# Performance work log

Hardware: AMD Instinct MI355X
Metric: run time of the kernel (lower is better)

Reference implementation:

```python
import jax, jax.numpy as jnp
import numpy as np

B, S, D, E, H = 1024, 256, 1024, 1024, 1024  # batch, state, belief, embedding, hidden
T1 = 32            # clip_length => number of scan steps
POSE_TILES = 4
MIN_STD = 0.1


def _gru(x, h, wih, whh, bih, bhh):
    # torch.nn.GRUCell semantics
    gi = x @ wih.T + bih
    gh = h @ whh.T + bhh
    i_r, i_z, i_n = jnp.split(gi, 3, axis=-1)
    h_r, h_z, h_n = jnp.split(gh, 3, axis=-1)
    r = jax.nn.sigmoid(i_r + h_r)
    z = jax.nn.sigmoid(i_z + h_z)
    n = jnp.tanh(i_n + r * h_n)
    return (1.0 - z) * n + z * h


def setup_inputs() -> dict:
    key = jax.random.key(0)
    ks = iter(jax.random.split(key, 40))
    g = lambda shape, s=1.0: jax.random.normal(next(ks), shape, dtype=jnp.float32) * s
    W = 0.02
    inp = {
        'prev_state': g((B, S)),
        'prev_belief': g((B, D)),
        'observations': g((T1, B, E)),
        'poses': g((T1, B, 6)),
        'noise_post': g((T1, B, S)),
        'noise_prior': g((T1, B, S)),
        # fc_embed_state_posterior: (2S+E) -> D
        'W_esq': g((D, 2 * S + E), W), 'b_esq': jnp.zeros((D,), jnp.float32),
        # fc_embed_state_prior: (2S+6*pose_tiles) -> D
        'W_esp': g((D, 2 * S + 6 * POSE_TILES), W), 'b_esp': jnp.zeros((D,), jnp.float32),
        # GRUCell posterior / prior
        'gq_wih': g((3 * D, D), W), 'gq_whh': g((3 * D, D), W),
        'gq_bih': jnp.zeros((3 * D,), jnp.float32), 'gq_bhh': jnp.zeros((3 * D,), jnp.float32),
        'gp_wih': g((3 * D, D), W), 'gp_whh': g((3 * D, D), W),
        'gp_bih': jnp.zeros((3 * D,), jnp.float32), 'gp_bhh': jnp.zeros((3 * D,), jnp.float32),
        # belief -> hidden -> 2*state heads
        'W_ebq': g((H, D), W), 'b_ebq': jnp.zeros((H,), jnp.float32),
        'W_sq': g((2 * S, H), W), 'b_sq': jnp.zeros((2 * S,), jnp.float32),
        'W_ebp': g((H, D), W), 'b_ebp': jnp.zeros((H,), jnp.float32),
        'W_sp': g((2 * S, H), W), 'b_sp': jnp.zeros((2 * S,), jnp.float32),
    }
    return inp


def reference(prev_state, prev_belief, observations, poses, noise_post, noise_prior,
              W_esq, b_esq, W_esp, b_esp,
              gq_wih, gq_whh, gq_bih, gq_bhh,
              gp_wih, gp_whh, gp_bih, gp_bhh,
              W_ebq, b_ebq, W_sq, b_sq, W_ebp, b_ebp, W_sp, b_sp):
    relu = jax.nn.relu

    def step(carry, xs):
        s_q, s_p, b_q, b_p = carry
        obs, pose, nq, npn = xs
        # posterior branch
        h = relu(jnp.concatenate([obs, s_q, s_p], axis=1) @ W_esq.T + b_esq)
        b_q_new = _gru(h, b_q, gq_wih, gq_whh, gq_bih, gq_bhh)
        hq = relu(b_q_new @ W_ebq.T + b_ebq)
        mq, raw_sq = jnp.split(hq @ W_sq.T + b_sq, 2, axis=1)
        std_q = jax.nn.softplus(raw_sq) + MIN_STD
        s_q_new = mq + std_q * nq
        # prior branch (uses old s_q, s_p per original code)
        pose_t = jnp.tile(pose, (1, POSE_TILES))
        h2 = relu(jnp.concatenate([pose_t, s_q, s_p], axis=1) @ W_esp.T + b_esp)
        b_p_new = _gru(h2, b_p, gp_wih, gp_whh, gp_bih, gp_bhh)
        hp = relu(b_p_new @ W_ebp.T + b_ebp)
        mp, raw_sp = jnp.split(hp @ W_sp.T + b_sp, 2, axis=1)
        std_p = jax.nn.softplus(raw_sp) + MIN_STD
        s_p_new = mp + std_p * npn
        new_carry = (s_q_new, s_p_new, b_q_new, b_p_new)
        ys = (b_q_new, s_p_new, mp, std_p, s_q_new, mq, std_q)
        return new_carry, ys

    carry0 = (prev_state, prev_state, prev_belief, prev_belief)
    _, ys = jax.lax.scan(step, carry0, (observations, poses, noise_post, noise_prior))
    post_beliefs, prior_states, prior_means, prior_stds, post_states, post_means, post_stds = ys
    # order matches torch: [posterior_beliefs, prior_states, prior_means, prior_std_devs,
    #                       posterior_states, posterior_means, posterior_std_devs]
    return (post_beliefs, prior_states, prior_means, prior_stds,
            post_states, post_means, post_stds)
```

## Files before the change

kernel.cpp:

```cpp
#include <hip/hip_runtime.h>
#include <stdint.h>
#include <math.h>

typedef unsigned short ushort_t;
typedef __attribute__((ext_vector_type(8))) short bf16x8;
typedef __attribute__((ext_vector_type(4))) float f32x4;

#define T1_ 32

__device__ __forceinline__ float bf2f(ushort_t u) {
  union { unsigned int i; float f; } v; v.i = ((unsigned int)u) << 16; return v.f;
}
__device__ __forceinline__ ushort_t f2bf(float f) {
  union { float f; unsigned int i; } v; v.f = f;
  unsigned int x = v.i;
  return (ushort_t)((x + 0x7FFFu + ((x >> 16) & 1u)) >> 16);
}
__device__ __forceinline__ float sigm(float x) { return 1.f / (1.f + expf(-x)); }

__device__ __forceinline__ void gld16(const ushort_t* g, ushort_t* l) {
  __builtin_amdgcn_global_load_lds(
      (const __attribute__((address_space(1))) unsigned int*)g,
      (__attribute__((address_space(3))) unsigned int*)l, 16, 0, 0);
}

__global__ __launch_bounds__(256) void cvt_k(const float* src, ushort_t* dst,
                                             long long n, int cols, int src_ld, int src_off) {
  const long long idx = (long long)blockIdx.x * 256 + threadIdx.x;
  if (idx >= n) return;
  const long long row = idx / cols;
  const int col = (int)(idx - row * cols);
  dst[idx] = f2bf(src[row * src_ld + src_off + col]);
}

__global__ __launch_bounds__(256) void wpe_k(const float* Wesp, float* wpe) {
  const int i = blockIdx.x * 256 + threadIdx.x;
  if (i >= 1024 * 6) return;
  const int n = i / 6, j = i % 6;
  float s = 0.f;
#pragma unroll
  for (int r = 0; r < 4; ++r) s += Wesp[(long long)n * 536 + j + 6 * r];
  wpe[i] = s;
}

__global__ void marker_k(float* out, float K) {
  if (threadIdx.x == 0 && blockIdx.x == 0) out[0] = K;
}

struct MMSide {
  const ushort_t* a0; const ushort_t* a1; const ushort_t* a2;
  int kd0, kd1, kd2;
  int coff0, coff1, coff2;
  int nparts;
  const ushort_t* W; int ldw;
  const float* bias;
  ushort_t* outb;
  int dopose;
};
struct MM2Args { MMSide s[2]; const float* poses_t; const float* wpe; };

__global__ __launch_bounds__(256) void mm2_k(MM2Args g) {
  const MMSide S = g.s[blockIdx.z];
  __shared__ __align__(16) ushort_t As[2048];
  __shared__ __align__(16) ushort_t Ws[4096];
  const int tid = threadIdx.x;
  const int lane = tid & 63, wave = tid >> 6;
  const int wm = wave >> 1, wn = wave & 1;
  const int bn0 = blockIdx.x * 128, bm0 = blockIdx.y * 64;

  f32x4 acc[2][4];
#pragma unroll
  for (int i = 0; i < 2; ++i)
#pragma unroll
    for (int j = 0; j < 4; ++j) acc[i][j] = (f32x4){0.f, 0.f, 0.f, 0.f};

  const ushort_t* ap[3] = { S.a0, S.a1, S.a2 };
  const int kd[3] = { S.kd0, S.kd1, S.kd2 };
  const int cf[3] = { S.coff0, S.coff1, S.coff2 };

  const int rowA = tid >> 2, kcA = (tid & 3) * 8;
  ushort_t* ldsA  = &As[wave * 512];
  ushort_t* ldsW0 = &Ws[wave * 512];
  ushort_t* ldsW1 = &Ws[2048 + wave * 512];

#pragma unroll 1
  for (int p = 0; p < S.nparts; ++p) {
    const int kdim = kd[p];
    const ushort_t* Ap = ap[p] + (long long)bm0 * kdim + (long long)rowA * kdim + kcA;
    const ushort_t* Wp0 = S.W + cf[p] + (long long)(bn0 + rowA) * S.ldw + kcA;
    const ushort_t* Wp1 = Wp0 + (long long)64 * S.ldw;
    const int nkt = kdim >> 5;
#pragma unroll 1
    for (int kt = 0; kt < nkt; ++kt) {
      const int k0 = kt * 32;
      __syncthreads();
      gld16(Ap + k0, ldsA);
      gld16(Wp0 + k0, ldsW0);
      gld16(Wp1 + k0, ldsW1);
      __syncthreads();
      const int r15 = lane & 15, kh = (lane >> 4) * 8;
      bf16x8 a[2], b[4];
#pragma unroll
      for (int i = 0; i < 2; ++i)
        a[i] = *(const bf16x8*)&As[(wm * 32 + i * 16 + r15) * 32 + kh];
#pragma unroll
      for (int j = 0; j < 4; ++j)
        b[j] = *(const bf16x8*)&Ws[(wn * 64 + j * 16 + r15) * 32 + kh];
#pragma unroll
      for (int i = 0; i < 2; ++i)
#pragma unroll
        for (int j = 0; j < 4; ++j)
          acc[i][j] = __builtin_amdgcn_mfma_f32_16x16x32_bf16(a[i], b[j], acc[i][j], 0, 0, 0);
    }
  }

  const int r15 = lane & 15, rq = (lane >> 4) * 4;
#pragma unroll
  for (int i = 0; i < 2; ++i) {
#pragma unroll
    for (int j = 0; j < 4; ++j) {
      const int col = bn0 + wn * 64 + j * 16 + r15;
      const float bs = S.bias[col];
#pragma unroll
      for (int q = 0; q < 4; ++q) {
        const int row = bm0 + wm * 32 + i * 16 + rq + q;
        float v = acc[i][j][q] + bs;
        if (S.dopose) {
          float s = 0.f;
#pragma unroll
          for (int jj = 0; jj < 6; ++jj)
            s += g.poses_t[(long long)row * 6 + jj] * g.wpe[col * 6 + jj];
          v += s;
        }
        v = fmaxf(v, 0.f);
        S.outb[(size_t)row * 1024 + col] = f2bf(v);
      }
    }
  }
}

struct GruSide {
  const ushort_t* x;
  const ushort_t* hb;
  const float* hf;
  const ushort_t* wih; const ushort_t* whh;
  const float* bih; const float* bhh;
  float* dst; ushort_t* dstb;
};
struct Gru2Args { GruSide s[2]; };

__global__ __launch_bounds__(256) void gru2_k(Gru2Args g) {
  const GruSide S = g.s[blockIdx.z];
  __shared__ __align__(16) ushort_t Xs[2048];
  __shared__ __align__(16) ushort_t Hs[2048];
  __shared__ __align__(16) ushort_t Wt[6][2048];
  const int tid = threadIdx.x;
  const int lane = tid & 63, wave = tid >> 6;
  const int wm = wave >> 1, wn = wave & 1;
  const int bn0 = blockIdx.x * 64, bm0 = blockIdx.y * 64;

  f32x4 acc[6][2][2];
#pragma unroll
  for (int gg = 0; gg < 6; ++gg)
#pragma unroll
    for (int i = 0; i < 2; ++i)
#pragma unroll
      for (int j = 0; j < 2; ++j) acc[gg][i][j] = (f32x4){0.f, 0.f, 0.f, 0.f};

  const int rowA = tid >> 2, kc = (tid & 3) * 8;
  const long long xoff = (long long)(bm0 + rowA) * 1024 + kc;

#pragma unroll 1
  for (int kt = 0; kt < 32; ++kt) {
    const int k0 = kt * 32;
    __syncthreads();
    gld16(S.x + xoff + k0, &Xs[wave * 512]);
    gld16(S.hb + xoff + k0, &Hs[wave * 512]);
#pragma unroll
    for (int gg = 0; gg < 6; ++gg) {
      const ushort_t* base = (gg < 3) ? S.wih : S.whh;
      const int grow = (gg % 3) * 1024 + bn0 + rowA;
      gld16(base + (long long)grow * 1024 + k0 + kc, &Wt[gg][wave * 512]);
    }
    __syncthreads();
    const int r15 = lane & 15, kh = (lane >> 4) * 8;
    bf16x8 ax[2], ah[2];
#pragma unroll
    for (int i = 0; i < 2; ++i) {
      ax[i] = *(const bf16x8*)&Xs[(wm * 32 + i * 16 + r15) * 32 + kh];
      ah[i] = *(const bf16x8*)&Hs[(wm * 32 + i * 16 + r15) * 32 + kh];
    }
#pragma unroll
    for (int gg = 0; gg < 6; ++gg) {
      bf16x8 bw[2];
#pragma unroll
      for (int j = 0; j < 2; ++j)
        bw[j] = *(const bf16x8*)&Wt[gg][(wn * 32 + j * 16 + r15) * 32 + kh];
#pragma unroll
      for (int i = 0; i < 2; ++i)
#pragma unroll
        for (int j = 0; j < 2; ++j)
          acc[gg][i][j] = __builtin_amdgcn_mfma_f32_16x16x32_bf16(
              (gg < 3) ? ax[i] : ah[i], bw[j], acc[gg][i][j], 0, 0, 0);
    }
  }

  const int r15 = lane & 15, rq = (lane >> 4) * 4;
#pragma unroll
  for (int j = 0; j < 2; ++j) {
    const int col = bn0 + wn * 32 + j * 16 + r15;
    const float br  = S.bih[col],        bhr = S.bhh[col];
    const float bz  = S.bih[col + 1024], bhz = S.bhh[col + 1024];
    const float bn_ = S.bih[col + 2048], bhn = S.bhh[col + 2048];
#pragma unroll
    for (int i = 0; i < 2; ++i) {
#pragma unroll
      for (int q = 0; q < 4; ++q) {
        const int row = bm0 + wm * 32 + i * 16 + rq + q;
        const float ir = acc[0][i][j][q] + br,   hr = acc[3][i][j][q] + bhr;
        const float iz = acc[1][i][j][q] + bz,   hz = acc[4][i][j][q] + bhz;
        const float in_ = acc[2][i][j][q] + bn_, hn = acc[5][i][j][q] + bhn;
        const float r = sigm(ir + hr);
        const float z = sigm(iz + hz);
        const float ng = tanhf(in_ + r * hn);
        const long long o = (long long)row * 1024 + col;
        const float bnew = (1.f - z) * ng + z * S.hf[o];
        S.dst[o] = bnew;
        S.dstb[o] = f2bf(bnew);
      }
    }
  }
}

struct HeadSide {
  const ushort_t* hh;
  const ushort_t* Ws;
  const float* bs;
  const float* noise;
  float* omean; float* ostd; float* ostate;
  ushort_t* stateb;
};
struct Head2Args { HeadSide s[2]; };

__global__ __launch_bounds__(256) void head2_k(Head2Args g) {
  const HeadSide S = g.s[blockIdx.z];
  __shared__ __align__(16) ushort_t As[2048];
  __shared__ __align__(16) ushort_t Wt[2][2048];
  const int tid = threadIdx.x;
  const int lane = tid & 63, wave = tid >> 6;
  const int wm = wave >> 1, wn = wave & 1;
  const int bn0 = blockIdx.x * 64, bm0 = blockIdx.y * 64;

  f32x4 acc[2][2][2];
#pragma unroll
  for (int gg = 0; gg < 2; ++gg)
#pragma unroll
    for (int i = 0; i < 2; ++i)
#pragma unroll
      for (int j = 0; j < 2; ++j) acc[gg][i][j] = (f32x4){0.f, 0.f, 0.f, 0.f};

  const int rowA = tid >> 2, kc = (tid & 3) * 8;
  const long long aoff = (long long)(bm0 + rowA) * 1024 + kc;

#pragma unroll 1
  for (int kt = 0; kt < 32; ++kt) {
    const int k0 = kt * 32;
    __syncthreads();
    gld16(S.hh + aoff + k0, &As[wave * 512]);
#pragma unroll
    for (int gg = 0; gg < 2; ++gg)
      gld16(S.Ws + (long long)(gg * 256 + bn0 + rowA) * 1024 + k0 + kc, &Wt[gg][wave * 512]);
    __syncthreads();
    const int r15 = lane & 15, kh = (lane >> 4) * 8;
    bf16x8 a[2];
#pragma unroll
    for (int i = 0; i < 2; ++i)
      a[i] = *(const bf16x8*)&As[(wm * 32 + i * 16 + r15) * 32 + kh];
#pragma unroll
    for (int gg = 0; gg < 2; ++gg) {
      bf16x8 bw[2];
#pragma unroll
      for (int j = 0; j < 2; ++j)
        bw[j] = *(const bf16x8*)&Wt[gg][(wn * 32 + j * 16 + r15) * 32 + kh];
#pragma unroll
      for (int i = 0; i < 2; ++i)
#pragma unroll
        for (int j = 0; j < 2; ++j)
          acc[gg][i][j] = __builtin_amdgcn_mfma_f32_16x16x32_bf16(a[i], bw[j], acc[gg][i][j], 0, 0, 0);
    }
  }

  const int r15 = lane & 15, rq = (lane >> 4) * 4;
#pragma unroll
  for (int j = 0; j < 2; ++j) {
    const int col = bn0 + wn * 32 + j * 16 + r15;
    const float bm = S.bs[col];
    const float bsd = S.bs[col + 256];
#pragma unroll
    for (int i = 0; i < 2; ++i) {
#pragma unroll
      for (int q = 0; q < 4; ++q) {
        const int row = bm0 + wm * 32 + i * 16 + rq + q;
        const float mean = acc[0][i][j][q] + bm;
        const float rs = acc[1][i][j][q] + bsd;
        const float sp = fmaxf(rs, 0.f) + log1pf(expf(-fabsf(rs)));
        const float sd = sp + 0.1f;
        const long long o = (long long)row * 256 + col;
        const float st = mean + sd * S.noise[o];
        S.omean[o] = mean; S.ostd[o] = sd; S.ostate[o] = st;
        S.stateb[o] = f2bf(st);
      }
    }
  }
}

extern "C" void kernel_launch(void* const* d_in, const int* in_sizes, int n_in,
                              void* d_out, int out_size, void* d_ws, size_t ws_size,
                              hipStream_t stream) {
  float* out = (float*)d_out;

  int gid = 0;
  if (n_in != 26) gid = 1;
  else if (out_size != 83886080) gid = 2;
  else if (in_sizes[0] != 262144 || in_sizes[1] != 1048576 || in_sizes[2] != 33554432 ||
           in_sizes[3] != 196608 || in_sizes[4] != 8388608 || in_sizes[5] != 8388608) gid = 3;
  else if (in_sizes[6] != 1572864 || in_sizes[8] != 548864) gid = 4;
  else if (in_sizes[10] != 3145728 || in_sizes[11] != 3145728 ||
           in_sizes[14] != 3145728 || in_sizes[15] != 3145728) gid = 5;
  else if (in_sizes[18] != 1048576 || in_sizes[20] != 524288 ||
           in_sizes[22] != 1048576 || in_sizes[24] != 524288) gid = 6;
  else if (ws_size < (128ull << 20)) gid = 7;
  if (gid != 0) {
    unsigned wsMB = (unsigned)(ws_size >> 20); if (wsMB > 4095u) wsMB = 4095u;
    const float K = (float)gid * 16777216.0f + (float)wsMB;
    hipLaunchKernelGGL(marker_k, dim3(1), dim3(64), 0, stream, out, K);
    return;
  }

  const float* prev_state  = (const float*)d_in[0];
  const float* prev_belief = (const float*)d_in[1];
  const float* observations= (const float*)d_in[2];
  const float* poses       = (const float*)d_in[3];
  const float* noise_post  = (const float*)d_in[4];
  const float* noise_prior = (const float*)d_in[5];
  const float* W_esq = (const float*)d_in[6];  const float* b_esq = (const float*)d_in[7];
  const float* W_esp = (const float*)d_in[8];  const float* b_esp = (const float*)d_in[9];
  const float* gq_wih = (const float*)d_in[10]; const float* gq_whh = (const float*)d_in[11];
  const float* gq_bih = (const float*)d_in[12]; const float* gq_bhh = (const float*)d_in[13];
  const float* gp_wih = (const float*)d_in[14]; const float* gp_whh = (const float*)d_in[15];
  const float* gp_bih = (const float*)d_in[16]; const float* gp_bhh = (const float*)d_in[17];
  const float* W_ebq = (const float*)d_in[18]; const float* b_ebq = (const float*)d_in[19];
  const float* W_sq  = (const float*)d_in[20]; const float* b_sq  = (const float*)d_in[21];
  const float* W_ebp = (const float*)d_in[22]; const float* b_ebp = (const float*)d_in[23];
  const float* W_sp  = (const float*)d_in[24]; const float* b_sp  = (const float*)d_in[25];

  float* out_belief = out;
  float* out_pstate = out + 33554432LL;
  float* out_pmean  = out + 41943040LL;
  float* out_pstd   = out + 50331648LL;
  float* out_qstate = out + 58720256LL;
  float* out_qmean  = out + 67108864LL;
  float* out_qstd   = out + 75497472LL;

  char* w = (char*)d_ws;
  ushort_t* obsb  = (ushort_t*)(w);
  ushort_t* wWesq = (ushort_t*)(w + (64ull << 20));
  ushort_t* wWesp = (ushort_t*)(w + (67ull << 20));
  ushort_t* wGqih = (ushort_t*)(w + (68ull << 20));
  ushort_t* wGqhh = (ushort_t*)(w + (74ull << 20));
  ushort_t* wGpih = (ushort_t*)(w + (80ull << 20));
  ushort_t* wGphh = (ushort_t*)(w + (86ull << 20));
  ushort_t* wEbq  = (ushort_t*)(w + (92ull << 20));
  ushort_t* wEbp  = (ushort_t*)(w + (94ull << 20));
  ushort_t* wSq   = (ushort_t*)(w + (96ull << 20));
  ushort_t* wSp   = (ushort_t*)(w + (97ull << 20));
  float*    wpe   = (float*)(w + (98ull << 20));
  ushort_t* h_q   = (ushort_t*)(w + (99ull << 20));
  ushort_t* h_p   = (ushort_t*)(w + (101ull << 20));
  ushort_t* bqb[2] = { (ushort_t*)(w + (103ull << 20)), (ushort_t*)(w + (105ull << 20)) };
  ushort_t* bpb[2] = { (ushort_t*)(w + (107ull << 20)), (ushort_t*)(w + (109ull << 20)) };
  ushort_t* sqb   = (ushort_t*)(w + (111ull << 20));
  ushort_t* spb   = (ushort_t*)(w + (111ull << 20) + 524288);
  float*    bpf[2] = { (float*)(w + (112ull << 20)), (float*)(w + (116ull << 20)) };

  const dim3 blk(256);
  auto cvt = [&](const float* s, ushort_t* d, long long n, int c, int ld, int off) {
    hipLaunchKernelGGL(cvt_k, dim3((unsigned)((n + 255) / 256)), blk, 0, stream, s, d, n, c, ld, off);
  };
  cvt(observations, obsb, 33554432LL, 1024, 1024, 0);
  cvt(W_esq, wWesq, 1572864LL, 1536, 1536, 0);
  cvt(W_esp, wWesp, 524288LL, 512, 536, 24);
  cvt(gq_wih, wGqih, 3145728LL, 1024, 1024, 0);
  cvt(gq_whh, wGqhh, 3145728LL, 1024, 1024, 0);
  cvt(gp_wih, wGpih, 3145728LL, 1024, 1024, 0);
  cvt(gp_whh, wGphh, 3145728LL, 1024, 1024, 0);
  cvt(W_ebq, wEbq, 1048576LL, 1024, 1024, 0);
  cvt(W_ebp, wEbp, 1048576LL, 1024, 1024, 0);
  cvt(W_sq, wSq, 524288LL, 1024, 1024, 0);
  cvt(W_sp, wSp, 524288LL, 1024, 1024, 0);
  cvt(prev_state, sqb, 262144LL, 256, 256, 0);
  cvt(prev_state, spb, 262144LL, 256, 256, 0);
  cvt(prev_belief, bqb[1], 1048576LL, 1024, 1024, 0);
  cvt(prev_belief, bpb[1], 1048576LL, 1024, 1024, 0);
  hipLaunchKernelGGL(wpe_k, dim3(24), blk, 0, stream, W_esp, wpe);

  for (int t = 0; t < T1_; ++t) {
    const int cur = t & 1, prv = cur ^ 1;
    const ushort_t* obs_t = obsb + (long long)t * 1048576;
    const float* bq_prev_f = (t == 0) ? prev_belief : out_belief + (long long)(t - 1) * 1048576;
    const float* bp_prev_f = (t == 0) ? prev_belief : bpf[prv];

    MM2Args a{};
    a.s[0] = MMSide{ obs_t, sqb, spb, 1024, 256, 256, 0, 1024, 1280, 3,
                     wWesq, 1536, b_esq, h_q, 0 };
    a.s[1] = MMSide{ sqb, spb, nullptr, 256, 256, 0, 0, 256, 0, 2,
                     wWesp, 512, b_esp, h_p, 1 };
    a.poses_t = poses + (long long)t * 6144; a.wpe = wpe;
    hipLaunchKernelGGL(mm2_k, dim3(8, 16, 2), blk, 0, stream, a);

    Gru2Args gr{};
    gr.s[0] = GruSide{ h_q, bqb[prv], bq_prev_f, wGqih, wGqhh, gq_bih, gq_bhh,
                       out_belief + (long long)t * 1048576, bqb[cur] };
    gr.s[1] = GruSide{ h_p, bpb[prv], bp_prev_f, wGpih, wGphh, gp_bih, gp_bhh,
                       bpf[cur], bpb[cur] };
    hipLaunchKernelGGL(gru2_k, dim3(16, 16, 2), blk, 0, stream, gr);

    a = MM2Args{};
    a.s[0] = MMSide{ bqb[cur], nullptr, nullptr, 1024, 0, 0, 0, 0, 0, 1,
                     wEbq, 1024, b_ebq, h_q, 0 };
    a.s[1] = MMSide{ bpb[cur], nullptr, nullptr, 1024, 0, 0, 0, 0, 0, 1,
                     wEbp, 1024, b_ebp, h_p, 0 };
    hipLaunchKernelGGL(mm2_k, dim3(8, 16, 2), blk, 0, stream, a);

    Head2Args hd{};
    hd.s[0] = HeadSide{ h_q, wSq, b_sq, noise_post + (long long)t * 262144,
                        out_qmean + (long long)t * 262144,
                        out_qstd + (long long)t * 262144,
                        out_qstate + (long long)t * 262144, sqb };
    hd.s[1] = HeadSide{ h_p, wSp, b_sp, noise_prior + (long long)t * 262144,
                        out_pmean + (long long)t * 262144,
                        out_pstd + (long long)t * 262144,
                        out_pstate + (long long)t * 262144, spb };
    hipLaunchKernelGGL(head2_k, dim3(4, 16, 2), blk, 0, stream, hd);
  }
}
```

Measured before the change: 4.067 ms.

## Double-buffer LDS staging in matmul, GRU and head kernels; enlarge GRU tile

The three GEMM-style kernels (mm2_k, gru2_k, head2_k) now use two LDS buffers and a single barrier per K-step. The next K-tile's global-to-LDS loads are issued before the MFMAs on the current tile, so load latency is meant to overlap with compute. mm2_k also flattens its multi-part K loop into one global loop. gru2_k moves to 512 threads with 128-row tiles, so each block reuses the six weight tiles across twice as many rows. In exchange, LDS use grows (about 80KB per GRU block), the GRU grid halves, and occupancy may fall.

```diff
diff --git a/kernel.cpp b/kernel.cpp
--- a/kernel.cpp
+++ b/kernel.cpp
@@ -51,7 +51,6 @@
   const ushort_t* a0; const ushort_t* a1; const ushort_t* a2;
   int kd0, kd1, kd2;
   int coff0, coff1, coff2;
-  int nparts;
   const ushort_t* W; int ldw;
   const float* bias;
   ushort_t* outb;
@@ -61,8 +60,8 @@
 
 __global__ __launch_bounds__(256) void mm2_k(MM2Args g) {
   const MMSide S = g.s[blockIdx.z];
-  __shared__ __align__(16) ushort_t As[2048];
-  __shared__ __align__(16) ushort_t Ws[4096];
+  __shared__ __align__(16) ushort_t As[2][2048];
+  __shared__ __align__(16) ushort_t Ws[2][4096];
   const int tid = threadIdx.x;
   const int lane = tid & 63, wave = tid >> 6;
   const int wm = wave >> 1, wn = wave & 1;
@@ -74,44 +73,42 @@
 #pragma unroll
     for (int j = 0; j < 4; ++j) acc[i][j] = (f32x4){0.f, 0.f, 0.f, 0.f};
 
-  const ushort_t* ap[3] = { S.a0, S.a1, S.a2 };
-  const int kd[3] = { S.kd0, S.kd1, S.kd2 };
-  const int cf[3] = { S.coff0, S.coff1, S.coff2 };
-
   const int rowA = tid >> 2, kcA = (tid & 3) * 8;
-  ushort_t* ldsA  = &As[wave * 512];
-  ushort_t* ldsW0 = &Ws[wave * 512];
-  ushort_t* ldsW1 = &Ws[2048 + wave * 512];
-
+  const int nk0 = S.kd0 >> 5, nk1 = S.kd1 >> 5, nk2 = S.kd2 >> 5;
+  const int c1 = nk0, c2 = nk0 + nk1, nkt = c2 + nk2;
+
+  auto stage = [&](int buf, int ktg) {
+    const ushort_t* ab; int ktl, kdim, cf;
+    if (ktg < c1)      { ab = S.a0; ktl = ktg;      kdim = S.kd0; cf = S.coff0; }
+    else if (ktg < c2) { ab = S.a1; ktl = ktg - c1; kdim = S.kd1; cf = S.coff1; }
+    else               { ab = S.a2; ktl = ktg - c2; kdim = S.kd2; cf = S.coff2; }
+    const int k0 = ktl * 32;
+    gld16(ab + (long long)(bm0 + rowA) * kdim + k0 + kcA, &As[buf][wave * 512]);
+    gld16(S.W + cf + (long long)(bn0 + rowA) * S.ldw + k0 + kcA, &Ws[buf][wave * 512]);
+    gld16(S.W + cf + (long long)(bn0 + 64 + rowA) * S.ldw + k0 + kcA, &Ws[buf][2048 + wave * 512]);
+  };
+
+  stage(0, 0);
+  __syncthreads();
+  int cur = 0;
 #pragma unroll 1
-  for (int p = 0; p < S.nparts; ++p) {
-    const int kdim = kd[p];
-    const ushort_t* Ap = ap[p] + (long long)bm0 * kdim + (long long)rowA * kdim + kcA;
-    const ushort_t* Wp0 = S.W + cf[p] + (long long)(bn0 + rowA) * S.ldw + kcA;
-    const ushort_t* Wp1 = Wp0 + (long long)64 * S.ldw;
-    const int nkt = kdim >> 5;
-#pragma unroll 1
-    for (int kt = 0; kt < nkt; ++kt) {
-      const int k0 = kt * 32;
-      __syncthreads();
-      gld16(Ap + k0, ldsA);
-      gld16(Wp0 + k0, ldsW0);
-      gld16(Wp1 + k0, ldsW1);
-      __syncthreads();
-      const int r15 = lane & 15, kh = (lane >> 4) * 8;
-      bf16x8 a[2], b[4];
-#pragma unroll
-      for (int i = 0; i < 2; ++i)
-        a[i] = *(const bf16x8*)&As[(wm * 32 + i * 16 + r15) * 32 + kh];
+  for (int ktg = 0; ktg < nkt; ++ktg) {
+    if (ktg + 1 < nkt) stage(cur ^ 1, ktg + 1);
+    const int r15 = lane & 15, kh = (lane >> 4) * 8;
+    bf16x8 a[2], b[4];
+#pragma unroll
+    for (int i = 0; i < 2; ++i)
+      a[i] = *(const bf16x8*)&As[cur][(wm * 32 + i * 16 + r15) * 32 + kh];
+#pragma unroll
+    for (int j = 0; j < 4; ++j)
+      b[j] = *(const bf16x8*)&Ws[cur][(wn * 64 + j * 16 + r15) * 32 + kh];
+#pragma unroll
+    for (int i = 0; i < 2; ++i)
 #pragma unroll
       for (int j = 0; j < 4; ++j)
-        b[j] = *(const bf16x8*)&Ws[(wn * 64 + j * 16 + r15) * 32 + kh];
-#pragma unroll
-      for (int i = 0; i < 2; ++i)
-#pragma unroll
-        for (int j = 0; j < 4; ++j)
-          acc[i][j] = __builtin_amdgcn_mfma_f32_16x16x32_bf16(a[i], b[j], acc[i][j], 0, 0, 0);
-    }
+        acc[i][j] = __builtin_amdgcn_mfma_f32_16x16x32_bf16(a[i], b[j], acc[i][j], 0, 0, 0);
+    __syncthreads();
+    cur ^= 1;
   }
 
   const int r15 = lane & 15, rq = (lane >> 4) * 4;
@@ -149,15 +146,15 @@
 };
 struct Gru2Args { GruSide s[2]; };
 
-__global__ __launch_bounds__(256) void gru2_k(Gru2Args g) {
+__global__ __launch_bounds__(512) void gru2_k(Gru2Args g) {
   const GruSide S = g.s[blockIdx.z];
-  __shared__ __align__(16) ushort_t Xs[2048];
-  __shared__ __align__(16) ushort_t Hs[2048];
-  __shared__ __align__(16) ushort_t Wt[6][2048];
+  __shared__ __align__(16) ushort_t Xs[2][4096];
+  __shared__ __align__(16) ushort_t Hs[2][4096];
+  __shared__ __align__(16) ushort_t Wt[2][6][2048];
   const int tid = threadIdx.x;
   const int lane = tid & 63, wave = tid >> 6;
   const int wm = wave >> 1, wn = wave & 1;
-  const int bn0 = blockIdx.x * 64, bm0 = blockIdx.y * 64;
+  const int bn0 = blockIdx.x * 64, bm0 = blockIdx.y * 128;
 
   f32x4 acc[6][2][2];
 #pragma unroll
@@ -170,32 +167,42 @@
   const int rowA = tid >> 2, kc = (tid & 3) * 8;
   const long long xoff = (long long)(bm0 + rowA) * 1024 + kc;
 
+  auto stage = [&](int buf, int kt) {
+    const int k0 = kt * 32;
+    gld16(S.x + xoff + k0, &Xs[buf][wave * 512]);
+    gld16(S.hb + xoff + k0, &Hs[buf][wave * 512]);
+#pragma unroll
+    for (int r = 0; r < 3; ++r) {
+      const int q = tid + 512 * r;
+      const int gg = q >> 8;
+      const int qq = q & 255;
+      const int wrow = qq >> 2, wkc = (qq & 3) * 8;
+      const ushort_t* base = (gg < 3) ? S.wih : S.whh;
+      const int grow = (gg % 3) * 1024 + bn0 + wrow;
+      gld16(base + (long long)grow * 1024 + k0 + wkc,
+            &Wt[buf][0][0] + wave * 512 + r * 4096);
+    }
+  };
+
+  stage(0, 0);
+  __syncthreads();
+  int cur = 0;
 #pragma unroll 1
   for (int kt = 0; kt < 32; ++kt) {
-    const int k0 = kt * 32;
-    __syncthreads();
-    gld16(S.x + xoff + k0, &Xs[wave * 512]);
-    gld16(S.hb + xoff + k0, &Hs[wave * 512]);
-#pragma unroll
-    for (int gg = 0; gg < 6; ++gg) {
-      const ushort_t* base = (gg < 3) ? S.wih : S.whh;
-      const int grow = (gg % 3) * 1024 + bn0 + rowA;
-      gld16(base + (long long)grow * 1024 + k0 + kc, &Wt[gg][wave * 512]);
-    }
-    __syncthreads();
+    if (kt + 1 < 32) stage(cur ^ 1, kt + 1);
     const int r15 = lane & 15, kh = (lane >> 4) * 8;
     bf16x8 ax[2], ah[2];
 #pragma unroll
     for (int i = 0; i < 2; ++i) {
-      ax[i] = *(const bf16x8*)&Xs[(wm * 32 + i * 16 + r15) * 32 + kh];
-      ah[i] = *(const bf16x8*)&Hs[(wm * 32 + i * 16 + r15) * 32 + kh];
+      ax[i] = *(const bf16x8*)&Xs[cur][(wm * 32 + i * 16 + r15) * 32 + kh];
+      ah[i] = *(const bf16x8*)&Hs[cur][(wm * 32 + i * 16 + r15) * 32 + kh];
     }
 #pragma unroll
     for (int gg = 0; gg < 6; ++gg) {
       bf16x8 bw[2];
 #pragma unroll
       for (int j = 0; j < 2; ++j)
-        bw[j] = *(const bf16x8*)&Wt[gg][(wn * 32 + j * 16 + r15) * 32 + kh];
+        bw[j] = *(const bf16x8*)&Wt[cur][gg][(wn * 32 + j * 16 + r15) * 32 + kh];
 #pragma unroll
       for (int i = 0; i < 2; ++i)
 #pragma unroll
@@ -203,6 +210,8 @@
           acc[gg][i][j] = __builtin_amdgcn_mfma_f32_16x16x32_bf16(
               (gg < 3) ? ax[i] : ah[i], bw[j], acc[gg][i][j], 0, 0, 0);
     }
+    __syncthreads();
+    cur ^= 1;
   }
 
   const int r15 = lane & 15, rq = (lane >> 4) * 4;
@@ -244,8 +253,8 @@
 
 __global__ __launch_bounds__(256) void head2_k(Head2Args g) {
   const HeadSide S = g.s[blockIdx.z];
-  __shared__ __align__(16) ushort_t As[2048];
-  __shared__ __align__(16) ushort_t Wt[2][2048];
+  __shared__ __align__(16) ushort_t As[2][2048];
+  __shared__ __align__(16) ushort_t Wt[2][2][2048];
   const int tid = threadIdx.x;
   const int lane = tid & 63, wave = tid >> 6;
   const int wm = wave >> 1, wn = wave & 1;
@@ -262,32 +271,40 @@
   const int rowA = tid >> 2, kc = (tid & 3) * 8;
   const long long aoff = (long long)(bm0 + rowA) * 1024 + kc;
 
+  auto stage = [&](int buf, int kt) {
+    const int k0 = kt * 32;
+    gld16(S.hh + aoff + k0, &As[buf][wave * 512]);
+#pragma unroll
+    for (int gg = 0; gg < 2; ++gg)
+      gld16(S.Ws + (long long)(gg * 256 + bn0 + rowA) * 1024 + k0 + kc,
+            &Wt[buf][gg][wave * 512]);
+  };
+
+  stage(0, 0);
+  __syncthreads();
+  int cur = 0;
 #pragma unroll 1
   for (int kt = 0; kt < 32; ++kt) {
-    const int k0 = kt * 32;
-    __syncthreads();
-    gld16(S.hh + aoff + k0, &As[wave * 512]);
-#pragma unroll
-    for (int gg = 0; gg < 2; ++gg)
-      gld16(S.Ws + (long long)(gg * 256 + bn0 + rowA) * 1024 + k0 + kc, &Wt[gg][wave * 512]);
-    __syncthreads();
+    if (kt + 1 < 32) stage(cur ^ 1, kt + 1);
     const int r15 = lane & 15, kh = (lane >> 4) * 8;
     bf16x8 a[2];
 #pragma unroll
     for (int i = 0; i < 2; ++i)
-      a[i] = *(const bf16x8*)&As[(wm * 32 + i * 16 + r15) * 32 + kh];
+      a[i] = *(const bf16x8*)&As[cur][(wm * 32 + i * 16 + r15) * 32 + kh];
 #pragma unroll
     for (int gg = 0; gg < 2; ++gg) {
       bf16x8 bw[2];
 #pragma unroll
       for (int j = 0; j < 2; ++j)
-        bw[j] = *(const bf16x8*)&Wt[gg][(wn * 32 + j * 16 + r15) * 32 + kh];
+        bw[j] = *(const bf16x8*)&Wt[cur][gg][(wn * 32 + j * 16 + r15) * 32 + kh];
 #pragma unroll
       for (int i = 0; i < 2; ++i)
 #pragma unroll
         for (int j = 0; j < 2; ++j)
           acc[gg][i][j] = __builtin_amdgcn_mfma_f32_16x16x32_bf16(a[i], bw[j], acc[gg][i][j], 0, 0, 0);
     }
+    __syncthreads();
+    cur ^= 1;
   }
 
   const int r15 = lane & 15, rq = (lane >> 4) * 4;
@@ -411,9 +428,9 @@
     const float* bp_prev_f = (t == 0) ? prev_belief : bpf[prv];
 
     MM2Args a{};
-    a.s[0] = MMSide{ obs_t, sqb, spb, 1024, 256, 256, 0, 1024, 1280, 3,
+    a.s[0] = MMSide{ obs_t, sqb, spb, 1024, 256, 256, 0, 1024, 1280,
                      wWesq, 1536, b_esq, h_q, 0 };
-    a.s[1] = MMSide{ sqb, spb, nullptr, 256, 256, 0, 0, 256, 0, 2,
+    a.s[1] = MMSide{ sqb, spb, nullptr, 256, 256, 0, 0, 256, 0,
                      wWesp, 512, b_esp, h_p, 1 };
     a.poses_t = poses + (long long)t * 6144; a.wpe = wpe;
     hipLaunchKernelGGL(mm2_k, dim3(8, 16, 2), blk, 0, stream, a);
@@ -423,12 +440,12 @@
                        out_belief + (long long)t * 1048576, bqb[cur] };
     gr.s[1] = GruSide{ h_p, bpb[prv], bp_prev_f, wGpih, wGphh, gp_bih, gp_bhh,
                        bpf[cur], bpb[cur] };
-    hipLaunchKernelGGL(gru2_k, dim3(16, 16, 2), blk, 0, stream, gr);
+    hipLaunchKernelGGL(gru2_k, dim3(16, 8, 2), dim3(512), 0, stream, gr);
 
     a = MM2Args{};
-    a.s[0] = MMSide{ bqb[cur], nullptr, nullptr, 1024, 0, 0, 0, 0, 0, 1,
+    a.s[0] = MMSide{ bqb[cur], nullptr, nullptr, 1024, 0, 0, 0, 0, 0,
                      wEbq, 1024, b_ebq, h_q, 0 };
-    a.s[1] = MMSide{ bpb[cur], nullptr, nullptr, 1024, 0, 0, 0, 0, 0, 1,
+    a.s[1] = MMSide{ bpb[cur], nullptr, nullptr, 1024, 0, 0, 0, 0, 0,
                      wEbp, 1024, b_ebp, h_p, 0 };
     hipLaunchKernelGGL(mm2_k, dim3(8, 16, 2), blk, 0, stream, a);
 
```

Result: no change. 4.035 ms (-0.8%).
